# Kernel tuning notes

Hardware: AMD Instinct MI355X
Metric: run time of the kernel (lower is better)

Reference implementation:

```python
import jax, jax.numpy as jnp
import numpy as np

FACTOR = 2  # upsample factor per spatial dim


def setup_inputs() -> dict:
    key = jax.random.key(0)
    k1, k2, k3 = jax.random.split(key, 3)
    B, C_in, C_out, H, W_ = 8, 128, 128, 64, 64
    x = jax.random.normal(k1, (B, C_in, H, W_), dtype=jnp.float32)
    # conv3x3 params (OIHW), fan-in scaled init like torch Conv2d default scale
    fan_in = C_in * 3 * 3
    W = jax.random.normal(k2, (C_out, C_in, 3, 3), dtype=jnp.float32) / np.sqrt(fan_in)
    b = jax.random.normal(k3, (C_out,), dtype=jnp.float32) * 0.01
    return {"x": x, "W": W, "b": b}


def reference(x, W, b):
    h = jnp.repeat(jnp.repeat(x, FACTOR, axis=2), FACTOR, axis=3)  # [B,C,2H,2W]
    # conv3x3: stride 1, padding 1
    out = jax.lax.conv_general_dilated(
        h, W,
        window_strides=(1, 1),
        padding=((1, 1), (1, 1)),
        dimension_numbers=("NCHW", "OIHW", "NCHW"),
    )
    return out + b[None, :, None, None]
```

## Files before the change

kernel.cpp:

```cpp
#include <hip/hip_runtime.h>
#include <stdint.h>

typedef short bf16x8 __attribute__((ext_vector_type(8)));
typedef float f32x4 __attribute__((ext_vector_type(4)));
typedef float f32x16 __attribute__((ext_vector_type(16)));

#define NCI 128
#define NCO 128
#define HIN 64
#define NB  8

__device__ __forceinline__ unsigned short f32_to_bf16(float f) {
    union { float f; uint32_t u; } v; v.f = f;
    return (unsigned short)((v.u + 0x7FFFu + ((v.u >> 16) & 1u)) >> 16);
}

__device__ __forceinline__ void gl_lds16(const void* g, void* l) {
    __builtin_amdgcn_global_load_lds(
        (const __attribute__((address_space(1))) unsigned int*)g,
        (__attribute__((address_space(3))) unsigned int*)l, 16, 0, 0);
}

__device__ __forceinline__ float weff_sum(const float* wp, int py, int px, int ty, int tx) {
    float s = 0.f;
    #pragma unroll
    for (int ky = 0; ky < 3; ++ky) {
        bool iy = (py == 0) ? (ty == 0 ? (ky == 0) : (ky >= 1))
                            : (ty == 0 ? (ky <= 1) : (ky == 2));
        if (!iy) continue;
        #pragma unroll
        for (int kx = 0; kx < 3; ++kx) {
            bool ix = (px == 0) ? (tx == 0 ? (kx == 0) : (kx >= 1))
                                : (tx == 0 ? (kx <= 1) : (kx == 2));
            if (ix) s += wp[ky * 3 + kx];
        }
    }
    return s;
}

__global__ __launch_bounds__(256) void prep_kernel(
        const float* __restrict__ W, const float* __restrict__ x,
        unsigned short* __restrict__ Aw9, unsigned short* __restrict__ xq) {
    if (blockIdx.x < 1024) {
        int idx = blockIdx.x * 256 + threadIdx.x;
        int e   = idx & 7;
        int l   = (idx >> 3) & 63;
        int fm  = (idx >> 9) & 1;
        int s   = (idx >> 10) & 31;
        int coh = (idx >> 15) & 1;
        int par = idx >> 16;
        int co = coh * 64 + fm * 32 + (l & 31);
        int k  = s * 16 + (l >> 5) * 8 + e;
        int tap = k >> 7, ci = k & 127;
        Aw9[idx] = f32_to_bf16(weff_sum(W + (co * NCI + ci) * 9,
                                        par >> 1, par & 1, tap >> 1, tap & 1));
    } else {
        const int bb = blockIdx.x - 1024;
        const int b = bb / 66, hp = bb % 66;
        const int t = threadIdx.x;
        if (hp == 0 || hp == 65) {
            bf16x8 z = (bf16x8){0, 0, 0, 0, 0, 0, 0, 0};
            for (int i = t; i < 1024; i += 256) {
                int g = i >> 8, rem = i & 255;
                int w = rem >> 2, q = rem & 3;
                *(bf16x8*)(xq + (((((size_t)(b * 4 + g)) * 66 + hp) * 64 + w) << 5) + q * 8) = z;
            }
            return;
        }
        const int h = hp - 1;
        const int w = t & 63, g = t >> 6;
        const float* src = x + ((size_t)(b * NCI + g * 32) * (HIN * HIN)) + h * HIN + w;
        unsigned short* dst = xq + (((((size_t)(b * 4 + g)) * 66 + hp) * 64 + w) << 5);
        #pragma unroll
        for (int q = 0; q < 4; ++q) {
            bf16x8 v;
            #pragma unroll
            for (int j = 0; j < 8; ++j)
                v[j] = (short)f32_to_bf16(src[(size_t)(q * 8 + j) * (HIN * HIN)]);
            *(bf16x8*)(dst + q * 8) = v;
        }
    }
}

__global__ __launch_bounds__(256, 2) void upconv17_kernel(
        const unsigned short* __restrict__ xq, const unsigned short* __restrict__ Aw9,
        const float* __restrict__ bv, float* __restrict__ out) {
    __shared__ __align__(16) unsigned short B_lds[40960];
    const int d = blockIdx.x;
    const int bi  = d & 7;
    const int py  = (d >> 3) & 1;
    const int px  = (d >> 4) & 1;
    const int coh = (d >> 5) & 1;
    const int ys  = d >> 6;
    const int tid = threadIdx.x, lane = tid & 63, ol = tid >> 6;
    const int l31 = lane & 31, lh = lane >> 5;
    const int par = py * 2 + px;

    #pragma unroll
    for (int i = 0; i < 20; ++i) {
        const int u = i * 256 + tid;
        const int qs = u & 15, cell = u >> 4;
        const int r = cell >> 6, w = cell & 63;
        const int q = qs ^ (w & 15);
        const int hp = ys * 4 + py + r;
        const unsigned short* gb = xq +
            (((((size_t)(bi * 4 + (q >> 2))) * 66 + hp) * 64 + w) << 5) + (q & 3) * 8;
        gl_lds16(gb, &B_lds[u * 8]);
    }

    const unsigned short* Ag = Aw9 + (((size_t)(par * 2 + coh)) << 15);
    bf16x8 Abuf[3][2];
    auto loadA = [&](bf16x8* Ad, int s) {
        const unsigned short* p = Ag + (s << 10) + lane * 8;
        Ad[0] = *(const bf16x8*)p;
        Ad[1] = *(const bf16x8*)(p + 512);
    };
    loadA(Abuf[0], 0);
    loadA(Abuf[1], 1);
    loadA(Abuf[2], 2);
    asm volatile("s_waitcnt vmcnt(0)" ::: "memory");
    __builtin_amdgcn_s_barrier();

    f32x16 acc[2][2];
    #pragma unroll
    for (int i = 0; i < 2; ++i)
        #pragma unroll
        for (int j = 0; j < 2; ++j)
            #pragma unroll
            for (int q = 0; q < 16; ++q)
                acc[i][j][q] = 0.f;

    #pragma unroll
    for (int s = 0; s < 32; ++s) {
        bf16x8* Ac = Abuf[s % 3];
        const int ty = s >> 4, tx = (s >> 3) & 1;
        const int q = (s & 7) * 2 + lh;
        const int r = ol + ty;
        __builtin_amdgcn_s_setprio(1);
        #pragma unroll
        for (int fn = 0; fn < 2; ++fn) {
            const int wr = fn * 32 + l31 + px + tx - 1;
            const bool valid = (unsigned)wr < 64u;
            const int w = valid ? wr : 0;
            const int qs = q ^ (w & 15);
            bf16x8 bfr = *(const bf16x8*)&B_lds[(((r << 6) + w) * 16 + qs) * 8];
            bfr = valid ? bfr : (bf16x8){0, 0, 0, 0, 0, 0, 0, 0};
            #pragma unroll
            for (int fm = 0; fm < 2; ++fm)
                acc[fm][fn] = __builtin_amdgcn_mfma_f32_32x32x16_bf16(
                    Ac[fm], bfr, acc[fm][fn], 0, 0, 0);
        }
        __builtin_amdgcn_s_setprio(0);
        if (s + 3 < 32) loadA(Abuf[s % 3], s + 3);
    }

    const int yy = 2 * (ys * 4 + ol) + py;
    #pragma unroll
    for (int fm = 0; fm < 2; ++fm) {
        #pragma unroll
        for (int fn = 0; fn < 2; ++fn) {
            const int xx = 2 * (fn * 32 + l31) + px;
            #pragma unroll
            for (int j = 0; j < 16; ++j) {
                const int row = (j & 3) + 8 * (j >> 2) + 4 * lh;
                const int co = coh * 64 + fm * 32 + row;
                out[(((size_t)(bi * NCO + co)) << 14) + yy * 128 + xx] =
                    acc[fm][fn][j] + bv[co];
            }
        }
    }
}

__global__ void weff_flat_kernel(const float* __restrict__ W,
                                 unsigned short* __restrict__ Aw) {
    int idx = blockIdx.x * 256 + threadIdx.x;
    int par = idx >> 16;
    int co  = (idx >> 9) & 127;
    int k   = idx & 511;
    int tap = k >> 7, ci = k & 127;
    Aw[idx] = f32_to_bf16(weff_sum(W + (co * NCI + ci) * 9,
                                   par >> 1, par & 1, tap >> 1, tap & 1));
}

__global__ __launch_bounds__(256) void upconv_fb_kernel(
        const float* __restrict__ x, const unsigned short* __restrict__ Aw,
        const float* __restrict__ bv, float* __restrict__ out) {
    __shared__ __align__(16) unsigned short A_lds[128 * 32];
    __shared__ __align__(16) unsigned short B_lds[128 * 32];
    const int par = blockIdx.y, py = par >> 1, px = par & 1;
    const int s0 = blockIdx.x * 128;
    const int bimg = s0 >> 12;
    const int oy0 = (s0 >> 6) & 63;
    const int tid = threadIdx.x;
    const int lane = tid & 63, wave = tid >> 6;
    const int wm = wave >> 1, wn = wave & 1;
    const float* xb = x + bimg * (NCI * HIN * HIN);
    f32x4 acc[4][4];
    #pragma unroll
    for (int i = 0; i < 4; ++i)
        #pragma unroll
        for (int j = 0; j < 4; ++j)
            acc[i][j] = (f32x4){0.f, 0.f, 0.f, 0.f};
    for (int kt = 0; kt < 16; ++kt) {
        const int tap = kt >> 2, ci0 = (kt & 3) * 32;
        const int ty = tap >> 1, tx = tap & 1;
        #pragma unroll
        for (int i = 0; i < 2; ++i) {
            int c = i * 256 + tid;
            *(bf16x8*)(&A_lds[c * 8]) = *(const bf16x8*)(Aw +
                ((par * 128 + (c >> 2)) * 512 + kt * 32 + (c & 3) * 8));
        }
        #pragma unroll
        for (int i = 0; i < 2; ++i) {
            int tsk = i * 256 + tid;
            int n = tsk & 127, kg = tsk >> 7;
            int r = n >> 6, ox = n & 63;
            int row = oy0 + r - 1 + py + ty;
            int col = ox - 1 + px + tx;
            bool ok = (row >= 0) & (row < HIN) & (col >= 0) & (col < HIN);
            const float* xp = xb + (((ci0 + kg * 8) * HIN + row) * HIN + col);
            bf16x8 v;
            #pragma unroll
            for (int q = 0; q < 8; ++q) {
                float f = ok ? xp[q * (HIN * HIN)] : 0.f;
                v[q] = (short)f32_to_bf16(f);
            }
            *(bf16x8*)(&B_lds[n * 32 + kg * 8]) = v;
        }
        __syncthreads();
        const int seg = (lane >> 4) * 8, rl2 = lane & 15;
        bf16x8 af[4], bfr[4];
        #pragma unroll
        for (int f = 0; f < 4; ++f)
            af[f] = *(const bf16x8*)(&A_lds[(wm * 64 + f * 16 + rl2) * 32 + seg]);
        #pragma unroll
        for (int f = 0; f < 4; ++f)
            bfr[f] = *(const bf16x8*)(&B_lds[(wn * 64 + f * 16 + rl2) * 32 + seg]);
        #pragma unroll
        for (int fm = 0; fm < 4; ++fm)
            #pragma unroll
            for (int fn = 0; fn < 4; ++fn)
                acc[fm][fn] = __builtin_amdgcn_mfma_f32_16x16x32_bf16(
                    af[fm], bfr[fn], acc[fm][fn], 0, 0, 0);
        __syncthreads();
    }
    #pragma unroll
    for (int fm = 0; fm < 4; ++fm) {
        const int co_b = wm * 64 + fm * 16 + (lane >> 4) * 4;
        float bias4[4];
        #pragma unroll
        for (int j = 0; j < 4; ++j) bias4[j] = bv[co_b + j];
        #pragma unroll
        for (int fn = 0; fn < 4; ++fn) {
            int n = wn * 64 + fn * 16 + (lane & 15);
            int s = s0 + n;
            int ox = s & 63, oy = (s >> 6) & 63, bi2 = s >> 12;
            int yy = 2 * oy + py, xx = 2 * ox + px;
            float* op = out + ((size_t)bi2 * 128 * 128 * 128) + (size_t)yy * 128 + xx;
            #pragma unroll
            for (int j = 0; j < 4; ++j)
                op[(size_t)(co_b + j) * (128 * 128)] = acc[fm][fn][j] + bias4[j];
        }
    }
}

extern "C" void kernel_launch(void* const* d_in, const int* in_sizes, int n_in,
                              void* d_out, int out_size, void* d_ws, size_t ws_size,
                              hipStream_t stream) {
    const float* x  = (const float*)d_in[0];
    const float* W  = (const float*)d_in[1];
    const float* bv = (const float*)d_in[2];
    float* out = (float*)d_out;
    unsigned short* Aw = (unsigned short*)d_ws;
    const size_t aw_bytes = (size_t)4 * 2 * 32 * 2 * 512 * sizeof(unsigned short);
    const size_t xq_bytes = (size_t)NB * 4 * 66 * 64 * 32 * sizeof(unsigned short);

    if (ws_size >= aw_bytes + xq_bytes) {
        unsigned short* xq = (unsigned short*)((char*)d_ws + aw_bytes);
        prep_kernel<<<1024 + 528, 256, 0, stream>>>(W, x, Aw, xq);
        upconv17_kernel<<<1024, 256, 0, stream>>>(xq, Aw, bv, out);
    } else {
        weff_flat_kernel<<<1024, 256, 0, stream>>>(W, Aw);
        upconv_fb_kernel<<<dim3(256, 4), 256, 0, stream>>>(x, Aw, bv, out);
    }
}
```

Before: 41.24 us.

## Pair column parities per block, shrink LDS tile, stage output through LDS

Each block now handles both column parities (px) across its four waves, each wave covering one px and one of two input rows, instead of one px and four rows. The LDS input tile therefore shrinks from 5 to 3 padded rows, which allows occupancy to rise to 3 blocks per CU. The epilogue writes accumulators into LDS so that even and odd output columns are interleaved, then emits coalesced 16-byte stores with the bias added. This replaces the earlier strided scalar stores, at the cost of extra barriers and LDS traffic in the epilogue.

Result: slower. 47.54 us (+15.3%).

```diff
diff --git a/kernel.cpp b/kernel.cpp
--- a/kernel.cpp
+++ b/kernel.cpp
@@ -82,27 +82,27 @@
     }
 }
 
-__global__ __launch_bounds__(256, 2) void upconv17_kernel(
+__global__ __launch_bounds__(256, 3) void upconv20_kernel(
         const unsigned short* __restrict__ xq, const unsigned short* __restrict__ Aw9,
         const float* __restrict__ bv, float* __restrict__ out) {
-    __shared__ __align__(16) unsigned short B_lds[40960];
+    __shared__ __align__(16) unsigned short B_lds[24576];
     const int d = blockIdx.x;
     const int bi  = d & 7;
     const int py  = (d >> 3) & 1;
-    const int px  = (d >> 4) & 1;
-    const int coh = (d >> 5) & 1;
-    const int ys  = d >> 6;
-    const int tid = threadIdx.x, lane = tid & 63, ol = tid >> 6;
+    const int coh = (d >> 4) & 1;
+    const int ys  = d >> 5;
+    const int tid = threadIdx.x, lane = tid & 63, wv = tid >> 6;
+    const int px = wv & 1, ol = wv >> 1;
     const int l31 = lane & 31, lh = lane >> 5;
     const int par = py * 2 + px;
 
     #pragma unroll
-    for (int i = 0; i < 20; ++i) {
+    for (int i = 0; i < 12; ++i) {
         const int u = i * 256 + tid;
         const int qs = u & 15, cell = u >> 4;
         const int r = cell >> 6, w = cell & 63;
         const int q = qs ^ (w & 15);
-        const int hp = ys * 4 + py + r;
+        const int hp = ys * 2 + py + r;
         const unsigned short* gb = xq +
             (((((size_t)(bi * 4 + (q >> 2))) * 66 + hp) * 64 + w) << 5) + (q & 3) * 8;
         gl_lds16(gb, &B_lds[u * 8]);
@@ -153,21 +153,39 @@
         __builtin_amdgcn_s_setprio(0);
         if (s + 3 < 32) loadA(Abuf[s % 3], s + 3);
     }
-
-    const int yy = 2 * (ys * 4 + ol) + py;
-    #pragma unroll
-    for (int fm = 0; fm < 2; ++fm) {
-        #pragma unroll
-        for (int fn = 0; fn < 2; ++fn) {
-            const int xx = 2 * (fn * 32 + l31) + px;
-            #pragma unroll
-            for (int j = 0; j < 16; ++j) {
-                const int row = (j & 3) + 8 * (j >> 2) + 4 * lh;
-                const int co = coh * 64 + fm * 32 + row;
-                out[(((size_t)(bi * NCO + co)) << 14) + yy * 128 + xx] =
-                    acc[fm][fn][j] + bv[co];
-            }
-        }
+    __syncthreads();
+
+    float* lf = (float*)B_lds;
+    const int co_rd = tid >> 2;
+    const int x32 = (tid & 3) * 32;
+    #pragma unroll
+    for (int rr = 0; rr < 2; ++rr) {
+        if (ol == rr) {
+            #pragma unroll
+            for (int fm = 0; fm < 2; ++fm)
+                #pragma unroll
+                for (int fn = 0; fn < 2; ++fn) {
+                    const int xx = 2 * (fn * 32 + l31) + px;
+                    #pragma unroll
+                    for (int j = 0; j < 16; ++j) {
+                        const int row = (j & 3) + 8 * (j >> 2) + 4 * lh;
+                        lf[(fm * 32 + row) * 132 + xx] = acc[fm][fn][j];
+                    }
+                }
+        }
+        __syncthreads();
+        const int co = coh * 64 + co_rd;
+        const float bb = bv[co];
+        const int yy = 2 * (ys * 2 + rr) + py;
+        float* op = out + (((size_t)(bi * NCO + co)) << 14) + yy * 128 + x32;
+        const float* sp = lf + co_rd * 132 + x32;
+        #pragma unroll
+        for (int qq = 0; qq < 8; ++qq) {
+            f32x4 v = *(const f32x4*)(sp + qq * 4);
+            v[0] += bb; v[1] += bb; v[2] += bb; v[3] += bb;
+            *(f32x4*)(op + qq * 4) = v;
+        }
+        if (rr == 0) __syncthreads();
     }
 }
 
@@ -186,7 +204,7 @@
         const float* __restrict__ x, const unsigned short* __restrict__ Aw,
         const float* __restrict__ bv, float* __restrict__ out) {
     __shared__ __align__(16) unsigned short A_lds[128 * 32];
-    __shared__ __align__(16) unsigned short B_lds[128 * 32];
+    __shared__ __align__(16) unsigned short B_lds2[128 * 32];
     const int par = blockIdx.y, py = par >> 1, px = par & 1;
     const int s0 = blockIdx.x * 128;
     const int bimg = s0 >> 12;
@@ -225,7 +243,7 @@
                 float f = ok ? xp[q * (HIN * HIN)] : 0.f;
                 v[q] = (short)f32_to_bf16(f);
             }
-            *(bf16x8*)(&B_lds[n * 32 + kg * 8]) = v;
+            *(bf16x8*)(&B_lds2[n * 32 + kg * 8]) = v;
         }
         __syncthreads();
         const int seg = (lane >> 4) * 8, rl2 = lane & 15;
@@ -235,7 +253,7 @@
             af[f] = *(const bf16x8*)(&A_lds[(wm * 64 + f * 16 + rl2) * 32 + seg]);
         #pragma unroll
         for (int f = 0; f < 4; ++f)
-            bfr[f] = *(const bf16x8*)(&B_lds[(wn * 64 + f * 16 + rl2) * 32 + seg]);
+            bfr[f] = *(const bf16x8*)(&B_lds2[(wn * 64 + f * 16 + rl2) * 32 + seg]);
         #pragma unroll
         for (int fm = 0; fm < 4; ++fm)
             #pragma unroll
@@ -278,7 +296,7 @@
     if (ws_size >= aw_bytes + xq_bytes) {
         unsigned short* xq = (unsigned short*)((char*)d_ws + aw_bytes);
         prep_kernel<<<1024 + 528, 256, 0, stream>>>(W, x, Aw, xq);
-        upconv17_kernel<<<1024, 256, 0, stream>>>(xq, Aw, bv, out);
+        upconv20_kernel<<<1024, 256, 0, stream>>>(xq, Aw, bv, out);
     } else {
         weff_flat_kernel<<<1024, 256, 0, stream>>>(W, Aw);
         upconv_fb_kernel<<<dim3(256, 4), 256, 0, stream>>>(x, Aw, bv, out);
```
